# Kernel optimization log

Measured on AMD Instinct MI355X. Metric: run time of the kernel, lower is better.

The kernel has to match this reference:

```python
import jax, jax.numpy as jnp
import numpy as np
import math

B, S, D, H = 4, 2048, 1024, 16
DK = D // H

def setup_inputs() -> dict:
    key = jax.random.key(0)
    ks = jax.random.split(key, 12)
    scale = 1.0 / math.sqrt(D)
    inp = {
        "query": jax.random.normal(ks[0], (B, S, D), jnp.float32),
        "key_": jax.random.normal(ks[1], (B, S, D), jnp.float32),
        "value": jax.random.normal(ks[2], (B, S, D), jnp.float32),
        "mask": jnp.broadcast_to(jnp.tril(jnp.ones((S, S), jnp.int32)), (B, S, S)),
        "Wq": jax.random.normal(ks[3], (D, D), jnp.float32) * scale,
        "bq": jnp.zeros((D,), jnp.float32),
        "Wk": jax.random.normal(ks[4], (D, D), jnp.float32) * scale,
        "bk": jnp.zeros((D,), jnp.float32),
        "Wv": jax.random.normal(ks[5], (D, D), jnp.float32) * scale,
        "bv": jnp.zeros((D,), jnp.float32),
        "Wo": jax.random.normal(ks[6], (D, D), jnp.float32) * scale,
        "bo": jnp.zeros((D,), jnp.float32),
    }
    return inp

def reference(query, key_, value, mask, Wq, bq, Wk, bk, Wv, bv, Wo, bo):
    # Linear projections (torch Linear: x @ W^T + b), split into heads [B,H,S,DK]
    def proj(x, W, b):
        y = jnp.einsum('bsd,ed->bse', x, W) + b
        return y.reshape(B, S, H, DK).transpose(0, 2, 1, 3)
    Q = proj(query, Wq, bq)
    K = proj(key_, Wk, bk)
    V = proj(value, Wv, bv)
    # scaled dot-product attention with additive mask-fill
    scores = jnp.einsum('bhqd,bhkd->bhqk', Q, K) / math.sqrt(DK)
    scores = jnp.where(mask[:, None, :, :] == 0, jnp.float32(-1e9), scores)
    attn = jax.nn.softmax(scores, axis=-1)  # dropout p=0.0 (eval) -> identity
    ctx = jnp.einsum('bhqk,bhkd->bhqd', attn, V)
    ctx = ctx.transpose(0, 2, 1, 3).reshape(B, S, D)
    out = jnp.einsum('bsd,ed->bse', ctx, Wo) + bo
    return out
```

## Files before the change

kernel.cpp:

```cpp
#include <hip/hip_runtime.h>
#include <hip/hip_bf16.h>
#include <cstdint>
#include <cstddef>

static constexpr int kB = 4, kS = 2048, kD = 1024, kH = 16, kDK = 64;
static constexpr int kM = kB * kS;

typedef __attribute__((ext_vector_type(8))) __bf16 bf16x8;
typedef __attribute__((ext_vector_type(4))) float f32x4;

#define MFMA_BF16(a, b, c) __builtin_amdgcn_mfma_f32_16x16x32_bf16((a), (b), (c), 0, 0, 0)

#define GLDS16(gp, lp)                                                        \
  __builtin_amdgcn_global_load_lds(                                           \
      (__attribute__((address_space(1))) void*)(gp),                          \
      (__attribute__((address_space(3))) void*)(lp), 16, 0, 0)

__device__ __forceinline__ bf16x8 cvt8(const float* s, int i) {
  const float4 a = ((const float4*)s)[i * 2 + 0];
  const float4 b = ((const float4*)s)[i * 2 + 1];
  bf16x8 o;
  o[0] = (__bf16)a.x; o[1] = (__bf16)a.y; o[2] = (__bf16)a.z; o[3] = (__bf16)a.w;
  o[4] = (__bf16)b.x; o[5] = (__bf16)b.y; o[6] = (__bf16)b.z; o[7] = (__bf16)b.w;
  return o;
}

__global__ __launch_bounds__(256) void cvt_f32_bf16(
    const float* __restrict__ src, __bf16* __restrict__ dst, int n8) {
  const int i = blockIdx.x * 256 + threadIdx.x;
  if (i >= n8) return;
  ((bf16x8*)dst)[i] = cvt8(src, i);
}

__global__ __launch_bounds__(256) void cvt_all(
    const float* __restrict__ q, const float* __restrict__ k,
    const float* __restrict__ v, const float* __restrict__ wq,
    const float* __restrict__ wk, const float* __restrict__ wv,
    const float* __restrict__ wo, __bf16* __restrict__ dq,
    __bf16* __restrict__ dk, __bf16* __restrict__ dv,
    __bf16* __restrict__ dwq, __bf16* __restrict__ dwk,
    __bf16* __restrict__ dwv, __bf16* __restrict__ dwo) {
  int bi = blockIdx.x;
  if (bi < 3 * 4096) {
    const int seg = bi >> 12;
    const int i = (bi & 4095) * 256 + threadIdx.x;
    const float* s = seg == 0 ? q : seg == 1 ? k : v;
    __bf16* d = seg == 0 ? dq : seg == 1 ? dk : dv;
    ((bf16x8*)d)[i] = cvt8(s, i);
  } else {
    bi -= 3 * 4096;
    const int seg = bi >> 9;
    const int i = (bi & 511) * 256 + threadIdx.x;
    const float* s = seg == 0 ? wq : seg == 1 ? wk : seg == 2 ? wv : wo;
    __bf16* d = seg == 0 ? dwq : seg == 1 ? dwk : seg == 2 ? dwv : dwo;
    ((bf16x8*)d)[i] = cvt8(s, i);
  }
}

template <typename OutT>
__device__ __forceinline__ void gemm_core(
    const __bf16* __restrict__ A, const __bf16* __restrict__ W,
    const float* __restrict__ bias, OutT* __restrict__ out, int mode, int bid,
    __bf16* As, __bf16* Ws) {
  const int tid = threadIdx.x;
  const int wave = tid >> 6, lane = tid & 63;
  const int col = lane & 15, quad = lane >> 4;
  const int m0 = (bid & 63) * 128;
  const int n0 = (bid >> 6) * 128;
  const int wr = (wave & 1) * 64, wc = (wave >> 1) * 64;

  f32x4 acc[4][4] = {};

  int srow[4], sgo[4];
#pragma unroll
  for (int i = 0; i < 4; ++i) {
    const int s = i * 256 + tid;
    srow[i] = s >> 3;
    sgo[i] = (((s & 7) ^ ((s >> 3) & 7))) * 8;
  }
  const int g0 = ((quad) ^ (col & 7)) * 16;
  const int g1 = ((quad + 4) ^ (col & 7)) * 16;

  for (int k0 = 0; k0 < 1024; k0 += 64) {
#pragma unroll
    for (int i = 0; i < 4; ++i) {
      GLDS16(A + (size_t)(m0 + srow[i]) * 1024 + k0 + sgo[i],
             (char*)As + i * 4096 + wave * 1024);
      GLDS16(W + (size_t)(n0 + srow[i]) * 1024 + k0 + sgo[i],
             (char*)Ws + i * 4096 + wave * 1024);
    }
    __syncthreads();
#pragma unroll
    for (int h = 0; h < 2; ++h) {
      const int go = h ? g1 : g0;
      bf16x8 af[4], wf[4];
#pragma unroll
      for (int t = 0; t < 4; ++t) {
        af[t] = *(const bf16x8*)((const char*)As + (wr + t * 16 + col) * 128 + go);
        wf[t] = *(const bf16x8*)((const char*)Ws + (wc + t * 16 + col) * 128 + go);
      }
#pragma unroll
      for (int rt = 0; rt < 4; ++rt)
#pragma unroll
        for (int ct = 0; ct < 4; ++ct)
          acc[rt][ct] = MFMA_BF16(af[rt], wf[ct], acc[rt][ct]);
    }
    __syncthreads();
  }

#pragma unroll
  for (int ct = 0; ct < 4; ++ct) {
    const int n = n0 + wc + ct * 16 + col;
    const float bb = bias[n];
#pragma unroll
    for (int rt = 0; rt < 4; ++rt) {
#pragma unroll
      for (int r = 0; r < 4; ++r) {
        const int m = m0 + wr + rt * 16 + quad * 4 + r;
        const float v = acc[rt][ct][r] + bb;
        size_t idx;
        if (mode == 0) {
          idx = (size_t)m * 1024 + n;
        } else {
          const int b = m >> 11, s = m & 2047;
          const int h = n >> 6, dk = n & 63;
          if (mode == 1)
            idx = ((size_t)(b * 16 + h) * 2048 + s) * 64 + dk;
          else
            idx = ((size_t)(b * 16 + h) * 64 + dk) * 2048 + s;
        }
        out[idx] = (OutT)v;
      }
    }
  }
}

template <int MODE, typename OutT>
__global__ __launch_bounds__(256) void gemm_one(
    const __bf16* __restrict__ A, const __bf16* __restrict__ W,
    const float* __restrict__ bias, OutT* __restrict__ out) {
  __shared__ __align__(16) __bf16 As[128 * 64];
  __shared__ __align__(16) __bf16 Ws[128 * 64];
  gemm_core<OutT>(A, W, bias, out, MODE, blockIdx.x, As, Ws);
}

__global__ __launch_bounds__(256) void gemm_qkv(
    const __bf16* __restrict__ Aq, const __bf16* __restrict__ Ak,
    const __bf16* __restrict__ Av, const __bf16* __restrict__ Wqb,
    const __bf16* __restrict__ Wkb, const __bf16* __restrict__ Wvb,
    const float* __restrict__ bq, const float* __restrict__ bk,
    const float* __restrict__ bv, __bf16* __restrict__ Qw,
    __bf16* __restrict__ Kw, __bf16* __restrict__ Vw) {
  __shared__ __align__(16) __bf16 As[128 * 64];
  __shared__ __align__(16) __bf16 Ws[128 * 64];
  const int seg = blockIdx.x >> 9;
  const int bid = blockIdx.x & 511;
  const __bf16* A = seg == 0 ? Aq : seg == 1 ? Ak : Av;
  const __bf16* W = seg == 0 ? Wqb : seg == 1 ? Wkb : Wvb;
  const float* bias = seg == 0 ? bq : seg == 1 ? bk : bv;
  __bf16* out = seg == 0 ? Qw : seg == 1 ? Kw : Vw;
  gemm_core<__bf16>(A, W, bias, out, seg == 2 ? 2 : 1, bid, As, Ws);
}

__global__ __launch_bounds__(256, 4) void flash_attn(
    const __bf16* __restrict__ Q, const __bf16* __restrict__ K,
    const __bf16* __restrict__ Vt, __bf16* __restrict__ ctx) {
  __shared__ __align__(16) __bf16 Ks[64 * 64];
  __shared__ __align__(16) __bf16 Vs[64 * 64];
  __shared__ __align__(16) __bf16 Pb[4][2][16 * 72];

  const int tid = threadIdx.x;
  const int wave = tid >> 6, lane = tid & 63;
  const int col = lane & 15, quad = lane >> 4;
  const int bh = blockIdx.x & 63;
  const int pair = blockIdx.x >> 6;
  const int b = bh >> 4, h = bh & 15;
  const int t_lo = pair, t_hi = 31 - pair;
  const int q0f[2] = {t_lo * 64 + wave * 16, t_hi * 64 + wave * 16};

  constexpr float SCL = 0.18033688011112042f;

  bf16x8 qf[2][2];
#pragma unroll
  for (int f = 0; f < 2; ++f) {
    const __bf16* Qp = Q + ((size_t)bh * kS + q0f[f] + col) * 64 + quad * 8;
    qf[f][0] = *(const bf16x8*)Qp;
    qf[f][1] = *(const bf16x8*)(Qp + 32);
  }

  f32x4 o[2][4] = {};
  f32x4 lacc[2] = {};
  bf16x8 ones;
#pragma unroll
  for (int i = 0; i < 8; ++i) ones[i] = (__bf16)1.0f;

  const __bf16* Kg = K + (size_t)bh * kS * 64;
  const __bf16* Vg = Vt + (size_t)bh * 64 * kS;

  const int row0 = tid >> 3, g0 = (tid & 7) ^ (row0 & 7);
  const int row1 = (256 + tid) >> 3, g1 = (tid & 7) ^ (row1 & 7);

  const int fgoff0 = ((quad) ^ (col & 7)) * 16;
  const int fgoff1 = ((quad + 4) ^ (col & 7)) * 16;
  const int maskbase = wave * 16 + quad * 4;

  __bf16* Pw0 = &Pb[wave][0][0];
  __bf16* Pw1 = &Pb[wave][1][0];
  const __bf16* Pr0 = Pw0 + col * 72 + quad * 8;
  const __bf16* Pr1 = Pw1 + col * 72 + quad * 8;

  auto stageK = [&](int c) {
    char* KsB = (char*)Ks + wave * 1024;
    GLDS16(Kg + (size_t)(c * 64 + row0) * 64 + g0 * 8, KsB);
    GLDS16(Kg + (size_t)(c * 64 + row1) * 64 + g1 * 8, KsB + 4096);
  };
  auto stageV = [&](int c) {
    char* VsB = (char*)Vs + wave * 1024;
    GLDS16(Vg + (size_t)row0 * kS + c * 64 + g0 * 8, VsB);
    GLDS16(Vg + (size_t)row1 * kS + c * 64 + g1 * 8, VsB + 4096);
  };

  auto body = [&](int c, bool lo, bool d0, bool d1, bool stage_next) {
    asm volatile("s_waitcnt vmcnt(2)" ::: "memory");
    __builtin_amdgcn_s_barrier();
    asm volatile("" ::: "memory");

    f32x4 s[2][4];
#pragma unroll
    for (int kt = 0; kt < 4; ++kt) {
      const char* kp = (const char*)Ks + (kt * 16 + col) * 128;
      const bf16x8 kf0 = *(const bf16x8*)(kp + fgoff0);
      const bf16x8 kf1 = *(const bf16x8*)(kp + fgoff1);
      f32x4 z = {};
      s[1][kt] = MFMA_BF16(qf[1][1], kf1, MFMA_BF16(qf[1][0], kf0, z));
      if (lo) s[0][kt] = MFMA_BF16(qf[0][1], kf1, MFMA_BF16(qf[0][0], kf0, z));
    }

    __builtin_amdgcn_s_barrier();
    asm volatile("" ::: "memory");
    if (stage_next) stageK(c + 1);

#pragma unroll
    for (int kt = 0; kt < 4; ++kt) {
#pragma unroll
      for (int r = 0; r < 4; ++r) {
        float pv1 = __builtin_amdgcn_exp2f(s[1][kt][r] * SCL);
        if (d1 && (kt * 16 + col > maskbase + r)) pv1 = 0.0f;
        Pw1[(quad * 4 + r) * 72 + kt * 16 + col] = (__bf16)pv1;
        if (lo) {
          float pv0 = __builtin_amdgcn_exp2f(s[0][kt][r] * SCL);
          if (d0 && (kt * 16 + col > maskbase + r)) pv0 = 0.0f;
          Pw0[(quad * 4 + r) * 72 + kt * 16 + col] = (__bf16)pv0;
        }
      }
    }
    __threadfence_block();

    if (stage_next)
      asm volatile("s_waitcnt vmcnt(2)" ::: "memory");
    else
      asm volatile("s_waitcnt vmcnt(0)" ::: "memory");
    __builtin_amdgcn_s_barrier();
    asm volatile("" ::: "memory");

    const bf16x8 pf1a = *(const bf16x8*)Pr1;
    const bf16x8 pf1b = *(const bf16x8*)(Pr1 + 32);
    bf16x8 pf0a = {}, pf0b = {};
    if (lo) {
      pf0a = *(const bf16x8*)Pr0;
      pf0b = *(const bf16x8*)(Pr0 + 32);
    }
#pragma unroll
    for (int dt = 0; dt < 4; ++dt) {
      const char* vp = (const char*)Vs + (dt * 16 + col) * 128;
      const bf16x8 vf0 = *(const bf16x8*)(vp + fgoff0);
      const bf16x8 vf1 = *(const bf16x8*)(vp + fgoff1);
      o[1][dt] = MFMA_BF16(pf1b, vf1, MFMA_BF16(pf1a, vf0, o[1][dt]));
      if (lo) o[0][dt] = MFMA_BF16(pf0b, vf1, MFMA_BF16(pf0a, vf0, o[0][dt]));
    }
    lacc[1] = MFMA_BF16(pf1b, ones, MFMA_BF16(pf1a, ones, lacc[1]));
    if (lo) lacc[0] = MFMA_BF16(pf0b, ones, MFMA_BF16(pf0a, ones, lacc[0]));

    __builtin_amdgcn_s_barrier();
    asm volatile("" ::: "memory");
    if (stage_next) stageV(c + 1);
  };

  stageK(0);
  stageV(0);
  for (int c = 0; c <= t_lo; ++c) body(c, true, c == t_lo, false, c < t_hi);
  for (int c = t_lo + 1; c <= t_hi; ++c)
    body(c, false, false, c == t_hi, c < t_hi);

#pragma unroll
  for (int f = 0; f < 2; ++f) {
#pragma unroll
    for (int r = 0; r < 4; ++r) {
      const float inv = 1.0f / lacc[f][r];
      const int srow = q0f[f] + quad * 4 + r;
      __bf16* cp = ctx + ((size_t)b * kS + srow) * kD + h * 64 + col;
#pragma unroll
      for (int dt = 0; dt < 4; ++dt)
        cp[dt * 16] = (__bf16)(o[f][dt][r] * inv);
    }
  }
}

extern "C" void kernel_launch(void* const* d_in, const int* in_sizes, int n_in,
                              void* d_out, int out_size, void* d_ws, size_t ws_size,
                              hipStream_t stream) {
  const float* query = (const float*)d_in[0];
  const float* key_  = (const float*)d_in[1];
  const float* value = (const float*)d_in[2];
  const float* Wq = (const float*)d_in[4];
  const float* bq = (const float*)d_in[5];
  const float* Wk = (const float*)d_in[6];
  const float* bk = (const float*)d_in[7];
  const float* Wv = (const float*)d_in[8];
  const float* bv = (const float*)d_in[9];
  const float* Wo = (const float*)d_in[10];
  const float* bo = (const float*)d_in[11];

  const size_t e = (size_t)kM * kD;
  const size_t w = (size_t)kD * kD;
  float* out = (float*)d_out;

  const size_t REQ = (6 * e + 4 * w) * sizeof(__bf16);

  if (ws_size >= REQ) {
    __bf16* Qw  = (__bf16*)d_ws;
    __bf16* Kw  = Qw + e;
    __bf16* Vw  = Kw + e;
    __bf16* Aq  = Vw + e;
    __bf16* Ak  = Aq + e;
    __bf16* Av  = Ak + e;
    __bf16* Wqb = Av + e;
    __bf16* Wkb = Wqb + w;
    __bf16* Wvb = Wkb + w;
    __bf16* Wob = Wvb + w;

    cvt_all<<<3 * 4096 + 4 * 512, 256, 0, stream>>>(
        query, key_, value, Wq, Wk, Wv, Wo, Aq, Ak, Av, Wqb, Wkb, Wvb, Wob);
    gemm_qkv<<<1536, 256, 0, stream>>>(Aq, Ak, Av, Wqb, Wkb, Wvb, bq, bk, bv,
                                       Qw, Kw, Vw);
    flash_attn<<<kB * kH * 16, 256, 0, stream>>>(Qw, Kw, Vw, Aq);
    gemm_one<0, float><<<512, 256, 0, stream>>>(Aq, Wob, bo, out);
  } else {
    __bf16* Qw = (__bf16*)d_ws;
    __bf16* Kw = Qw + e;
    __bf16* Vw = Kw + e;
    __bf16* Ab = Vw + e;
    __bf16* Wb = Ab + e;

    const int actg = (int)(e / 8 / 256);
    const int wg = (int)(w / 8 / 256);
    cvt_f32_bf16<<<actg, 256, 0, stream>>>(query, Ab, (int)(e / 8));
    cvt_f32_bf16<<<wg, 256, 0, stream>>>(Wq, Wb, (int)(w / 8));
    gemm_one<1, __bf16><<<512, 256, 0, stream>>>(Ab, Wb, bq, Qw);
    cvt_f32_bf16<<<actg, 256, 0, stream>>>(key_, Ab, (int)(e / 8));
    cvt_f32_bf16<<<wg, 256, 0, stream>>>(Wk, Wb, (int)(w / 8));
    gemm_one<1, __bf16><<<512, 256, 0, stream>>>(Ab, Wb, bk, Kw);
    cvt_f32_bf16<<<actg, 256, 0, stream>>>(value, Ab, (int)(e / 8));
    cvt_f32_bf16<<<wg, 256, 0, stream>>>(Wv, Wb, (int)(w / 8));
    gemm_one<2, __bf16><<<512, 256, 0, stream>>>(Ab, Wb, bv, Vw);
    flash_attn<<<kB * kH * 16, 256, 0, stream>>>(Qw, Kw, Vw, Ab);
    cvt_f32_bf16<<<wg, 256, 0, stream>>>(Wo, Wb, (int)(w / 8));
    gemm_one<0, float><<<512, 256, 0, stream>>>(Ab, Wb, bo, out);
  }
}
```

Before: 344.7 us.

## Fuse fp32-to-bf16 conversion into GEMM loads and drop separate cvt kernel

The separate conversion kernel is removed. The projection GEMMs now read fp32 activations and weights directly into registers, convert them to bf16 and store them to LDS, with a register prefetch of the next K tile. The flash-attention kernel writes its context in fp32 so the output GEMM can use the same fp32-input path. This removes a full read/write pass over all inputs and shrinks the workspace, but it doubles global read bytes inside the GEMMs, re-converts each tile many times across blocks, and replaces async global-to-LDS loads with register staging.

```diff
diff --git a/kernel.cpp b/kernel.cpp
--- a/kernel.cpp
+++ b/kernel.cpp
@@ -16,13 +16,17 @@
       (__attribute__((address_space(1))) void*)(gp),                          \
       (__attribute__((address_space(3))) void*)(lp), 16, 0, 0)
 
-__device__ __forceinline__ bf16x8 cvt8(const float* s, int i) {
-  const float4 a = ((const float4*)s)[i * 2 + 0];
-  const float4 b = ((const float4*)s)[i * 2 + 1];
+__device__ __forceinline__ bf16x8 to8(const float4& a, const float4& b) {
   bf16x8 o;
   o[0] = (__bf16)a.x; o[1] = (__bf16)a.y; o[2] = (__bf16)a.z; o[3] = (__bf16)a.w;
   o[4] = (__bf16)b.x; o[5] = (__bf16)b.y; o[6] = (__bf16)b.z; o[7] = (__bf16)b.w;
   return o;
+}
+
+__device__ __forceinline__ bf16x8 cvt8(const float* s, int i) {
+  const float4 a = ((const float4*)s)[i * 2 + 0];
+  const float4 b = ((const float4*)s)[i * 2 + 1];
+  return to8(a, b);
 }
 
 __global__ __launch_bounds__(256) void cvt_f32_bf16(
@@ -32,34 +36,9 @@
   ((bf16x8*)dst)[i] = cvt8(src, i);
 }
 
-__global__ __launch_bounds__(256) void cvt_all(
-    const float* __restrict__ q, const float* __restrict__ k,
-    const float* __restrict__ v, const float* __restrict__ wq,
-    const float* __restrict__ wk, const float* __restrict__ wv,
-    const float* __restrict__ wo, __bf16* __restrict__ dq,
-    __bf16* __restrict__ dk, __bf16* __restrict__ dv,
-    __bf16* __restrict__ dwq, __bf16* __restrict__ dwk,
-    __bf16* __restrict__ dwv, __bf16* __restrict__ dwo) {
-  int bi = blockIdx.x;
-  if (bi < 3 * 4096) {
-    const int seg = bi >> 12;
-    const int i = (bi & 4095) * 256 + threadIdx.x;
-    const float* s = seg == 0 ? q : seg == 1 ? k : v;
-    __bf16* d = seg == 0 ? dq : seg == 1 ? dk : dv;
-    ((bf16x8*)d)[i] = cvt8(s, i);
-  } else {
-    bi -= 3 * 4096;
-    const int seg = bi >> 9;
-    const int i = (bi & 511) * 256 + threadIdx.x;
-    const float* s = seg == 0 ? wq : seg == 1 ? wk : seg == 2 ? wv : wo;
-    __bf16* d = seg == 0 ? dwq : seg == 1 ? dwk : seg == 2 ? dwv : dwo;
-    ((bf16x8*)d)[i] = cvt8(s, i);
-  }
-}
-
 template <typename OutT>
-__device__ __forceinline__ void gemm_core(
-    const __bf16* __restrict__ A, const __bf16* __restrict__ W,
+__device__ __forceinline__ void gemm_core_f(
+    const float* __restrict__ A, const float* __restrict__ W,
     const float* __restrict__ bias, OutT* __restrict__ out, int mode, int bid,
     __bf16* As, __bf16* Ws) {
   const int tid = threadIdx.x;
@@ -76,20 +55,40 @@
   for (int i = 0; i < 4; ++i) {
     const int s = i * 256 + tid;
     srow[i] = s >> 3;
-    sgo[i] = (((s & 7) ^ ((s >> 3) & 7))) * 8;
+    sgo[i] = ((s & 7) ^ ((s >> 3) & 7)) * 8;
   }
   const int g0 = ((quad) ^ (col & 7)) * 16;
   const int g1 = ((quad + 4) ^ (col & 7)) * 16;
 
+  float4 ra[4][2], rw[4][2];
+
+  auto issue = [&](int k0) {
+#pragma unroll
+    for (int i = 0; i < 4; ++i) {
+      const float4* pa =
+          (const float4*)(A + (size_t)(m0 + srow[i]) * 1024 + k0 + sgo[i]);
+      const float4* pw =
+          (const float4*)(W + (size_t)(n0 + srow[i]) * 1024 + k0 + sgo[i]);
+      ra[i][0] = pa[0];
+      ra[i][1] = pa[1];
+      rw[i][0] = pw[0];
+      rw[i][1] = pw[1];
+    }
+  };
+
+  issue(0);
   for (int k0 = 0; k0 < 1024; k0 += 64) {
 #pragma unroll
     for (int i = 0; i < 4; ++i) {
-      GLDS16(A + (size_t)(m0 + srow[i]) * 1024 + k0 + sgo[i],
-             (char*)As + i * 4096 + wave * 1024);
-      GLDS16(W + (size_t)(n0 + srow[i]) * 1024 + k0 + sgo[i],
-             (char*)Ws + i * 4096 + wave * 1024);
-    }
-    __syncthreads();
+      *(bf16x8*)((char*)As + i * 4096 + tid * 16) = to8(ra[i][0], ra[i][1]);
+      *(bf16x8*)((char*)Ws + i * 4096 + tid * 16) = to8(rw[i][0], rw[i][1]);
+    }
+    asm volatile("s_waitcnt lgkmcnt(0)" ::: "memory");
+    __builtin_amdgcn_s_barrier();
+    asm volatile("" ::: "memory");
+
+    if (k0 < 960) issue(k0 + 64);
+
 #pragma unroll
     for (int h = 0; h < 2; ++h) {
       const int go = h ? g1 : g0;
@@ -105,7 +104,8 @@
         for (int ct = 0; ct < 4; ++ct)
           acc[rt][ct] = MFMA_BF16(af[rt], wf[ct], acc[rt][ct]);
     }
-    __syncthreads();
+    __builtin_amdgcn_s_barrier();
+    asm volatile("" ::: "memory");
   }
 
 #pragma unroll
@@ -135,6 +135,110 @@
   }
 }
 
+__global__ __launch_bounds__(256, 2) void gemm_qkv_f(
+    const float* __restrict__ Aq, const float* __restrict__ Ak,
+    const float* __restrict__ Av, const float* __restrict__ Wq,
+    const float* __restrict__ Wk, const float* __restrict__ Wv,
+    const float* __restrict__ bq, const float* __restrict__ bk,
+    const float* __restrict__ bv, __bf16* __restrict__ Qw,
+    __bf16* __restrict__ Kw, __bf16* __restrict__ Vw) {
+  __shared__ __align__(16) __bf16 As[128 * 64];
+  __shared__ __align__(16) __bf16 Ws[128 * 64];
+  const int seg = blockIdx.x >> 9;
+  const int bid = blockIdx.x & 511;
+  const float* A = seg == 0 ? Aq : seg == 1 ? Ak : Av;
+  const float* W = seg == 0 ? Wq : seg == 1 ? Wk : Wv;
+  const float* bias = seg == 0 ? bq : seg == 1 ? bk : bv;
+  __bf16* out = seg == 0 ? Qw : seg == 1 ? Kw : Vw;
+  gemm_core_f<__bf16>(A, W, bias, out, seg == 2 ? 2 : 1, bid, As, Ws);
+}
+
+__global__ __launch_bounds__(256, 2) void gemm_out_f(
+    const float* __restrict__ A, const float* __restrict__ W,
+    const float* __restrict__ bias, float* __restrict__ out) {
+  __shared__ __align__(16) __bf16 As[128 * 64];
+  __shared__ __align__(16) __bf16 Ws[128 * 64];
+  gemm_core_f<float>(A, W, bias, out, 0, blockIdx.x, As, Ws);
+}
+
+template <typename OutT>
+__device__ __forceinline__ void gemm_core(
+    const __bf16* __restrict__ A, const __bf16* __restrict__ W,
+    const float* __restrict__ bias, OutT* __restrict__ out, int mode, int bid,
+    __bf16* As, __bf16* Ws) {
+  const int tid = threadIdx.x;
+  const int wave = tid >> 6, lane = tid & 63;
+  const int col = lane & 15, quad = lane >> 4;
+  const int m0 = (bid & 63) * 128;
+  const int n0 = (bid >> 6) * 128;
+  const int wr = (wave & 1) * 64, wc = (wave >> 1) * 64;
+
+  f32x4 acc[4][4] = {};
+
+  int srow[4], sgo[4];
+#pragma unroll
+  for (int i = 0; i < 4; ++i) {
+    const int s = i * 256 + tid;
+    srow[i] = s >> 3;
+    sgo[i] = (((s & 7) ^ ((s >> 3) & 7))) * 8;
+  }
+  const int g0 = ((quad) ^ (col & 7)) * 16;
+  const int g1 = ((quad + 4) ^ (col & 7)) * 16;
+
+  for (int k0 = 0; k0 < 1024; k0 += 64) {
+#pragma unroll
+    for (int i = 0; i < 4; ++i) {
+      GLDS16(A + (size_t)(m0 + srow[i]) * 1024 + k0 + sgo[i],
+             (char*)As + i * 4096 + wave * 1024);
+      GLDS16(W + (size_t)(n0 + srow[i]) * 1024 + k0 + sgo[i],
+             (char*)Ws + i * 4096 + wave * 1024);
+    }
+    __syncthreads();
+#pragma unroll
+    for (int h = 0; h < 2; ++h) {
+      const int go = h ? g1 : g0;
+      bf16x8 af[4], wf[4];
+#pragma unroll
+      for (int t = 0; t < 4; ++t) {
+        af[t] = *(const bf16x8*)((const char*)As + (wr + t * 16 + col) * 128 + go);
+        wf[t] = *(const bf16x8*)((const char*)Ws + (wc + t * 16 + col) * 128 + go);
+      }
+#pragma unroll
+      for (int rt = 0; rt < 4; ++rt)
+#pragma unroll
+        for (int ct = 0; ct < 4; ++ct)
+          acc[rt][ct] = MFMA_BF16(af[rt], wf[ct], acc[rt][ct]);
+    }
+    __syncthreads();
+  }
+
+#pragma unroll
+  for (int ct = 0; ct < 4; ++ct) {
+    const int n = n0 + wc + ct * 16 + col;
+    const float bb = bias[n];
+#pragma unroll
+    for (int rt = 0; rt < 4; ++rt) {
+#pragma unroll
+      for (int r = 0; r < 4; ++r) {
+        const int m = m0 + wr + rt * 16 + quad * 4 + r;
+        const float v = acc[rt][ct][r] + bb;
+        size_t idx;
+        if (mode == 0) {
+          idx = (size_t)m * 1024 + n;
+        } else {
+          const int b = m >> 11, s = m & 2047;
+          const int h = n >> 6, dk = n & 63;
+          if (mode == 1)
+            idx = ((size_t)(b * 16 + h) * 2048 + s) * 64 + dk;
+          else
+            idx = ((size_t)(b * 16 + h) * 64 + dk) * 2048 + s;
+        }
+        out[idx] = (OutT)v;
+      }
+    }
+  }
+}
+
 template <int MODE, typename OutT>
 __global__ __launch_bounds__(256) void gemm_one(
     const __bf16* __restrict__ A, const __bf16* __restrict__ W,
@@ -144,27 +248,10 @@
   gemm_core<OutT>(A, W, bias, out, MODE, blockIdx.x, As, Ws);
 }
 
-__global__ __launch_bounds__(256) void gemm_qkv(
-    const __bf16* __restrict__ Aq, const __bf16* __restrict__ Ak,
-    const __bf16* __restrict__ Av, const __bf16* __restrict__ Wqb,
-    const __bf16* __restrict__ Wkb, const __bf16* __restrict__ Wvb,
-    const float* __restrict__ bq, const float* __restrict__ bk,
-    const float* __restrict__ bv, __bf16* __restrict__ Qw,
-    __bf16* __restrict__ Kw, __bf16* __restrict__ Vw) {
-  __shared__ __align__(16) __bf16 As[128 * 64];
-  __shared__ __align__(16) __bf16 Ws[128 * 64];
-  const int seg = blockIdx.x >> 9;
-  const int bid = blockIdx.x & 511;
-  const __bf16* A = seg == 0 ? Aq : seg == 1 ? Ak : Av;
-  const __bf16* W = seg == 0 ? Wqb : seg == 1 ? Wkb : Wvb;
-  const float* bias = seg == 0 ? bq : seg == 1 ? bk : bv;
-  __bf16* out = seg == 0 ? Qw : seg == 1 ? Kw : Vw;
-  gemm_core<__bf16>(A, W, bias, out, seg == 2 ? 2 : 1, bid, As, Ws);
-}
-
+template <typename CtxT>
 __global__ __launch_bounds__(256, 4) void flash_attn(
     const __bf16* __restrict__ Q, const __bf16* __restrict__ K,
-    const __bf16* __restrict__ Vt, __bf16* __restrict__ ctx) {
+    const __bf16* __restrict__ Vt, CtxT* __restrict__ ctx) {
   __shared__ __align__(16) __bf16 Ks[64 * 64];
   __shared__ __align__(16) __bf16 Vs[64 * 64];
   __shared__ __align__(16) __bf16 Pb[4][2][16 * 72];
@@ -298,10 +385,10 @@
     for (int r = 0; r < 4; ++r) {
       const float inv = 1.0f / lacc[f][r];
       const int srow = q0f[f] + quad * 4 + r;
-      __bf16* cp = ctx + ((size_t)b * kS + srow) * kD + h * 64 + col;
+      CtxT* cp = ctx + ((size_t)b * kS + srow) * kD + h * 64 + col;
 #pragma unroll
       for (int dt = 0; dt < 4; ++dt)
-        cp[dt * 16] = (__bf16)(o[f][dt][r] * inv);
+        cp[dt * 16] = (CtxT)(o[f][dt][r] * inv);
     }
   }
 }
@@ -325,26 +412,18 @@
   const size_t w = (size_t)kD * kD;
   float* out = (float*)d_out;
 
-  const size_t REQ = (6 * e + 4 * w) * sizeof(__bf16);
+  const size_t REQ = 3 * e * sizeof(__bf16) + e * sizeof(float);
 
   if (ws_size >= REQ) {
-    __bf16* Qw  = (__bf16*)d_ws;
-    __bf16* Kw  = Qw + e;
-    __bf16* Vw  = Kw + e;
-    __bf16* Aq  = Vw + e;
-    __bf16* Ak  = Aq + e;
-    __bf16* Av  = Ak + e;
-    __bf16* Wqb = Av + e;
-    __bf16* Wkb = Wqb + w;
-    __bf16* Wvb = Wkb + w;
-    __bf16* Wob = Wvb + w;
-
-    cvt_all<<<3 * 4096 + 4 * 512, 256, 0, stream>>>(
-        query, key_, value, Wq, Wk, Wv, Wo, Aq, Ak, Av, Wqb, Wkb, Wvb, Wob);
-    gemm_qkv<<<1536, 256, 0, stream>>>(Aq, Ak, Av, Wqb, Wkb, Wvb, bq, bk, bv,
-                                       Qw, Kw, Vw);
-    flash_attn<<<kB * kH * 16, 256, 0, stream>>>(Qw, Kw, Vw, Aq);
-    gemm_one<0, float><<<512, 256, 0, stream>>>(Aq, Wob, bo, out);
+    __bf16* Qw = (__bf16*)d_ws;
+    __bf16* Kw = Qw + e;
+    __bf16* Vw = Kw + e;
+    float* Ctx = (float*)(Vw + e);
+
+    gemm_qkv_f<<<1536, 256, 0, stream>>>(query, key_, value, Wq, Wk, Wv,
+                                         bq, bk, bv, Qw, Kw, Vw);
+    flash_attn<float><<<kB * kH * 16, 256, 0, stream>>>(Qw, Kw, Vw, Ctx);
+    gemm_out_f<<<512, 256, 0, stream>>>(Ctx, Wo, bo, out);
   } else {
     __bf16* Qw = (__bf16*)d_ws;
     __bf16* Kw = Qw + e;
@@ -363,7 +442,7 @@
     cvt_f32_bf16<<<actg, 256, 0, stream>>>(value, Ab, (int)(e / 8));
     cvt_f32_bf16<<<wg, 256, 0, stream>>>(Wv, Wb, (int)(w / 8));
     gemm_one<2, __bf16><<<512, 256, 0, stream>>>(Ab, Wb, bv, Vw);
-    flash_attn<<<kB * kH * 16, 256, 0, stream>>>(Qw, Kw, Vw, Ab);
+    flash_attn<__bf16><<<kB * kH * 16, 256, 0, stream>>>(Qw, Kw, Vw, Ab);
     cvt_f32_bf16<<<wg, 256, 0, stream>>>(Wo, Wb, (int)(w / 8));
     gemm_one<0, float><<<512, 256, 0, stream>>>(Ab, Wb, bo, out);
   }
```

After: 395.8 us. 1.15x slower.
